# Kernel tuning notes

Measured on AMD Instinct MI355X. Metric: run time of the kernel, lower is better.

## Reference

```python
import jax, jax.numpy as jnp
import numpy as np

B, S, V, E, H, F, L = 64, 32, 10000, 512, 512, 2048, 2
D = E + H  # concat(x, h) size; embedding_size == hidden_size so all layers share shapes


def setup_inputs() -> dict:
    key = jax.random.key(0)
    ks = jax.random.split(key, 10)

    def w(k, shape, fan):
        return jax.random.normal(k, shape, jnp.float32) / jnp.sqrt(jnp.float32(fan))

    tokens = jax.random.randint(ks[0], (B, S), 0, V)
    cnn_features = jax.random.normal(ks[1], (B, F), jnp.float32)
    emb = w(ks[2], (V, E), E)
    w_in = w(ks[3], (F, H), F)
    b_in = jnp.zeros((H,), jnp.float32)
    w_r = w(ks[4], (L, D, H), D)
    b_r = jnp.zeros((L, 1, H), jnp.float32)
    w_u = w(ks[5], (L, D, H), D)
    b_u = jnp.zeros((L, 1, H), jnp.float32)
    w_h = w(ks[6], (L, D, H), D)
    b_h = jnp.zeros((L, 1, H), jnp.float32)
    w_out = w(ks[7], (H, V), H)
    b_out = jnp.zeros((V,), jnp.float32)
    return dict(tokens=tokens, cnn_features=cnn_features, emb=emb, w_in=w_in, b_in=b_in,
                w_r=w_r, b_r=b_r, w_u=w_u, b_u=b_u, w_h=w_h, b_h=b_h,
                w_out=w_out, b_out=b_out)


def reference(tokens, cnn_features, emb, w_in, b_in, w_r, b_r, w_u, b_u, w_h, b_h, w_out, b_out):
    x = emb[tokens]                                   # [B, S, E]
    h0 = cnn_features @ w_in + b_in                   # [B, H] initial hidden state from CNN features
    seq = x
    for l in range(L):
        Wr, br = w_r[l], b_r[l]
        Wu, bu = w_u[l], b_u[l]
        Wh, bh = w_h[l], b_h[l]

        def step(h, xt):
            # xt: [B, D_in], h: [B, H] -- same GRU math as GRUCell.forward, batched
            xh = jnp.concatenate([xt, h], axis=-1)
            r = jax.nn.sigmoid(xh @ Wr + br)
            h_tilde = jnp.tanh(jnp.concatenate([xt, r * h], axis=-1) @ Wh + bh)
            u = jax.nn.sigmoid(xh @ Wu + bu)
            h_new = h * u + (1.0 - u) * h_tilde
            return h_new, h_new

        _, ys = jax.lax.scan(step, h0, jnp.swapaxes(seq, 0, 1))  # scan over time
        seq = jnp.swapaxes(ys, 0, 1)                  # [B, S, H]
    logits = seq @ w_out + b_out                      # [B, S, V]
    return logits
```

## Files before the change

### kernel.cpp

```cpp
#include <hip/hip_runtime.h>
#include <hip/hip_bf16.h>

typedef __hip_bfloat16 bf16;
typedef __attribute__((ext_vector_type(8))) short bf16x8s;
typedef __attribute__((ext_vector_type(4))) float f32x4;
typedef __attribute__((ext_vector_type(4))) int i32x4;

#define NB 64
#define NS 32
#define NV 10000
#define NE 512
#define NH 512
#define NF 2048
#define ND 1024

static __device__ __forceinline__ float bf2f(bf16 x) { return __bfloat162float(x); }
static __device__ __forceinline__ bf16 f2bf(float x) { return __float2bfloat16(x); }
static __device__ __forceinline__ short bfbits(float x) { bf16 h = f2bf(x); return *(short*)&h; }
static __device__ __forceinline__ f32x4 mfma16(bf16x8s a, bf16x8s b, f32x4 c) {
  return __builtin_amdgcn_mfma_f32_16x16x32_bf16(a, b, c, 0, 0, 0);
}

static __device__ __forceinline__ i32x4 ld16_sc(const void* p) {
  i32x4 r;
  asm volatile("global_load_dwordx4 %0, %1, off sc0 sc1" : "=v"(r) : "v"(p) : "memory");
  return r;
}
static __device__ __forceinline__ void st16_sc(void* p, i32x4 v) {
  asm volatile("global_store_dwordx4 %0, %1, off sc0 sc1" :: "v"(p), "v"(v) : "memory");
}
static __device__ __forceinline__ void stud_sc(void* p, unsigned v) {
  asm volatile("global_store_dword %0, %1, off sc0 sc1" :: "v"(p), "v"(v) : "memory");
}
static __device__ __forceinline__ void wait_vm0() {
  asm volatile("s_waitcnt vmcnt(0)" ::: "memory");
  __builtin_amdgcn_sched_barrier(0);
}
static __device__ __forceinline__ unsigned min4u(i32x4 a) {
  return min(min((unsigned)a[0], (unsigned)a[1]), min((unsigned)a[2], (unsigned)a[3]));
}

__device__ __forceinline__ f32x4 wave_tile16(const bf16* A, const bf16* BT,
                                             int lda, int K, int m0, int n0) {
  int lane = threadIdx.x & 63;
  int r = lane & 15, g = lane >> 4;
  const bf16* ap = A + (size_t)(m0 + r) * lda + g * 8;
  const bf16* bp = BT + (size_t)(n0 + r) * K + g * 8;
  f32x4 acc = {0.f, 0.f, 0.f, 0.f};
#pragma unroll 4
  for (int k = 0; k < K; k += 32) {
    bf16x8s a = *(const bf16x8s*)(ap + k);
    bf16x8s b = *(const bf16x8s*)(bp + k);
    acc = mfma16(a, b, acc);
  }
  return acc;
}

__global__ void k_setup(const float* __restrict__ cnn, bf16* __restrict__ cnn_b,
                        const float* __restrict__ w_in, bf16* __restrict__ w_in_T,
                        const float* __restrict__ w_r, const float* __restrict__ w_u,
                        const float* __restrict__ w_h, bf16* __restrict__ ruhT,
                        bf16* __restrict__ hhT, bf16* __restrict__ xT,
                        const float* __restrict__ br, const float* __restrict__ bu,
                        const float* __restrict__ bh, float* __restrict__ bias) {
  const int bid = blockIdx.x;
  if (bid < 512) {
    int i = bid * 256 + threadIdx.x;
    cnn_b[i] = f2bf(cnn[i]);
    return;
  }
  if (bid < 4608) {
    const float* src; bf16* dst; int n0, k0, N;
    if (bid < 1536) {
      int b = bid - 512;
      n0 = (b & 15) * 32; k0 = (b >> 4) * 32; N = NH;
      src = w_in; dst = w_in_T;
      __shared__ float tile[32][33];
      int tx = threadIdx.x & 31, ty = threadIdx.x >> 5;
      for (int i = ty; i < 32; i += 8)
        tile[i][tx] = src[(size_t)(k0 + i) * N + n0 + tx];
      __syncthreads();
      for (int i = ty; i < 32; i += 8)
        dst[(size_t)(n0 + i) * NF + k0 + tx] = f2bf(tile[tx][i]);
      return;
    }
    int b = bid - 1536;
    int z = b >> 8, xy = b & 255;
    int l = z / 6, q = z % 6;
    const float* srcs[6] = {
      w_r + (size_t)l * ND * NH + (size_t)512 * NH,
      w_u + (size_t)l * ND * NH + (size_t)512 * NH,
      w_h + (size_t)l * ND * NH + (size_t)512 * NH,
      w_r + (size_t)l * ND * NH,
      w_u + (size_t)l * ND * NH,
      w_h + (size_t)l * ND * NH };
    bf16* dsts[6] = {
      ruhT + (size_t)l * 1024 * 512,
      ruhT + (size_t)l * 1024 * 512 + 512 * 512,
      hhT  + (size_t)l * 512 * 512,
      xT   + (size_t)l * 1536 * 512,
      xT   + (size_t)l * 1536 * 512 + 512 * 512,
      xT   + (size_t)l * 1536 * 512 + 1024 * 512 };
    src = srcs[q]; dst = dsts[q];
    n0 = (xy & 15) * 32; k0 = (xy >> 4) * 32;
    __shared__ float tile[32][33];
    int tx = threadIdx.x & 31, ty = threadIdx.x >> 5;
    for (int i = ty; i < 32; i += 8)
      tile[i][tx] = src[(size_t)(k0 + i) * NH + n0 + tx];
    __syncthreads();
    for (int i = ty; i < 32; i += 8)
      dst[(size_t)(n0 + i) * NH + k0 + tx] = f2bf(tile[tx][i]);
    return;
  }
  int i = (bid - 4608) * 256 + threadIdx.x;
  if (i < 3072) {
    int l = i / 1536, c = i % 1536;
    const float* s = (c < 512) ? (br + l * 512 + c)
                   : (c < 1024 ? (bu + l * 512 + (c - 512)) : (bh + l * 512 + (c - 1024)));
    bias[i] = *s;
  }
}

__global__ void k_gemm_h0(const bf16* __restrict__ A, const bf16* __restrict__ BT,
                          const float* __restrict__ bias,
                          float* __restrict__ h0f, bf16* __restrict__ h0b) {
  int wid = blockIdx.x * 4 + (threadIdx.x >> 6);
  int mt = wid & 3, nt = wid >> 2;
  f32x4 acc = wave_tile16(A, BT, NF, NF, mt * 16, nt * 16);
  int lane = threadIdx.x & 63;
  int cl = lane & 15, g = lane >> 4;
  int col = nt * 16 + cl;
  float bv = bias[col];
#pragma unroll
  for (int j = 0; j < 4; j++) {
    int row = mt * 16 + g * 4 + j;
    float v = acc[j] + bv;
    h0f[(size_t)row * NH + col] = v;
    h0b[(size_t)row * NH + col] = f2bf(v);
  }
}

__global__ __launch_bounds__(512, 1)
void k_gru2(const bf16* __restrict__ w_ruh, const bf16* __restrict__ w_hh,
            const bf16* __restrict__ w_x, const float* __restrict__ bias3,
            const float* __restrict__ h0f, const bf16* __restrict__ h0b,
            const int* __restrict__ tokens, const float* __restrict__ emb,
            bf16* __restrict__ seq0, bf16* __restrict__ seq1,
            bf16* __restrict__ rh_all, float* __restrict__ pre,
            unsigned* __restrict__ flags, const float* __restrict__ w_out,
            const float* __restrict__ b_out, float* __restrict__ out) {
  __shared__ char lds[40960];
  const int tid = threadIdx.x;
  const int lane = tid & 63;
  const int wv = tid >> 6;
  const int cl = lane & 15, g4 = lane >> 4;
  const int bid = blockIdx.x;
  const int in0 = lane * 16;
  const int dsw = in0 ^ ((wv & 7) << 4);

  auto stage = [&](char* dst, const char* srcbase, int rstr) {
    i32x4 v0 = ld16_sc(srcbase + (size_t)wv * rstr + in0);
    i32x4 v1 = ld16_sc(srcbase + (size_t)(wv + 8) * rstr + in0);
    wait_vm0();
    *(i32x4*)(dst + wv * 1024 + dsw) = v0;
    *(i32x4*)(dst + (wv + 8) * 1024 + dsw) = v1;
  };
  auto afrag = [&](const char* panel, int kk) {
    return *(const bf16x8s*)(panel + cl * 1024 + ((kk * 64 + g4 * 16) ^ ((cl & 7) << 4)));
  };
  auto poll8 = [&](const unsigned* f, unsigned tgt) {
    if (tid == 0) {
      for (;;) {
        i32x4 a = ld16_sc(f);
        i32x4 b = ld16_sc(f + 4);
        wait_vm0();
        if (min(min4u(a), min4u(b)) >= tgt) break;
        __builtin_amdgcn_s_sleep(1);
      }
    }
    __syncthreads();
    __builtin_amdgcn_sched_barrier(0);
  };
  auto poll32 = [&](const unsigned* f, unsigned tgt) {
    if (tid == 0) {
      for (;;) {
        i32x4 a0 = ld16_sc(f),      a1 = ld16_sc(f + 4),  a2 = ld16_sc(f + 8),
              a3 = ld16_sc(f + 12), a4 = ld16_sc(f + 16), a5 = ld16_sc(f + 20),
              a6 = ld16_sc(f + 24), a7 = ld16_sc(f + 28);
        wait_vm0();
        unsigned mn = min(min(min(min4u(a0), min4u(a1)), min(min4u(a2), min4u(a3))),
                          min(min(min4u(a4), min4u(a5)), min(min4u(a6), min4u(a7))));
        if (mn >= tgt) break;
        __builtin_amdgcn_s_sleep(1);
      }
    }
    __syncthreads();
    __builtin_amdgcn_sched_barrier(0);
  };

  if (bid < 64) {
    const int l = bid >> 5, wg5 = bid & 31, mt = wg5 & 3, ng = wg5 >> 2;
    const bool is_u = (wv >= 4);
    const int wsub = wv & 3;
    const int c = (ng * 4 + wsub) * 16 + cl;
    const int colA = is_u ? 512 + c : c;
    char* hp = lds;
    char* rp = lds + 16384;
    float* ul = (float*)(lds + 32768);
    char* rout = lds + 36864;
    char* hout = lds + 38912;

    unsigned* f_h  = flags + (l * 4 + mt) * 32;
    unsigned* f_rh = flags + 256 + (l * 4 + mt) * 32;
    unsigned* f_pre = flags + 512 + (l * 4 + mt) * 32;

    bf16* seql = l ? seq1 : seq0;
    bf16* rh = rh_all + (size_t)l * 64 * 512;
    float* prel = pre + (size_t)l * 4 * 1536 * 64;

    bf16x8s bwA[16];
    { const bf16* pa = w_ruh + (size_t)l * 1024 * 512 + (size_t)colA * NH + g4 * 8;
#pragma unroll
      for (int k = 0; k < 16; k++) bwA[k] = *(const bf16x8s*)(pa + k * 32); }
    bf16x8s bwB[16];
    float h_reg[4];
    if (!is_u) {
      const bf16* pb = w_hh + (size_t)l * 512 * 512 + (size_t)c * NH + g4 * 8;
#pragma unroll
      for (int k = 0; k < 16; k++) bwB[k] = *(const bf16x8s*)(pb + k * 32);
#pragma unroll
      for (int j = 0; j < 4; j++)
        h_reg[j] = h0f[(size_t)(mt * 16 + g4 * 4 + j) * NH + c];
    }

    for (int t = 0; t < NS; t++) {
      if (tid == 0) {
        for (;;) {
          i32x4 p0 = ld16_sc(f_pre), p1 = ld16_sc(f_pre + 4), p2 = ld16_sc(f_pre + 8);
          i32x4 h0_, h1_;
          if (t) { h0_ = ld16_sc(f_h); h1_ = ld16_sc(f_h + 4); }
          wait_vm0();
          unsigned mnp = min(min(min4u(p0), min4u(p1)), min4u(p2));
          bool ok = mnp >= (unsigned)(t + 1);
          if (t) ok = ok && (min(min4u(h0_), min4u(h1_)) >= (unsigned)t);
          if (ok) break;
          __builtin_amdgcn_s_sleep(1);
        }
      }
      __syncthreads();
      __builtin_amdgcn_sched_barrier(0);
      const int slot = t & 3;
      i32x4 pv1 = ld16_sc(prel + ((size_t)(slot * 1536 + colA) * 64 + mt * 16 + g4 * 4));
      i32x4 pv2 = {0, 0, 0, 0};
      if (!is_u)
        pv2 = ld16_sc(prel + ((size_t)(slot * 1536 + 1024 + c) * 64 + mt * 16 + g4 * 4));
      if (t == 0) stage(hp, (const char*)(h0b + (size_t)mt * 16 * NH), 1024);
      else        stage(hp, (const char*)seql + ((size_t)(mt * 16) * NS + (t - 1)) * 1024,
                        NS * 1024);
      __syncthreads();
      f32x4 pA = *(f32x4*)&pv1;
      f32x4 pB = *(f32x4*)&pv2;
      {
        f32x4 acc = {0.f, 0.f, 0.f, 0.f};
#pragma unroll
        for (int kk = 0; kk < 16; kk++) acc = mfma16(afrag(hp, kk), bwA[kk], acc);
#pragma unroll
        for (int j = 0; j < 4; j++) {
          float gate = 1.f / (1.f + expf(-(acc[j] + pA[j])));
          if (is_u) {
            ul[(g4 * 4 + j) * 64 + wsub * 16 + cl] = gate;
          } else {
            bf16 o = f2bf(gate * h_reg[j]);
            *(unsigned short*)(rout + (g4 * 4 + j) * 128 + (wsub * 16 + cl) * 2)
              = *(unsigned short*)&o;
          }
        }
      }
      __syncthreads();
      {
        if (tid < 128) {
          int row = tid >> 3, ch = tid & 7;
          i32x4 v = *(i32x4*)(rout + row * 128 + ch * 16);
          st16_sc((char*)rh + (((size_t)(mt * 16 + row)) * NH + ng * 64 + ch * 8) * 2, v);
        }
        wait_vm0();
        __syncthreads();
        if (tid == 0) stud_sc(f_rh + ng, (unsigned)(t + 1));
      }
      poll8(f_rh, (unsigned)(t + 1));
      stage(rp, (const char*)(rh + (size_t)mt * 16 * NH), 1024);
      __syncthreads();
      if (!is_u) {
        f32x4 acc = {0.f, 0.f, 0.f, 0.f};
#pragma unroll
        for (int kk = 0; kk < 16; kk++) acc = mfma16(afrag(rp, kk), bwB[kk], acc);
#pragma unroll
        for (int j = 0; j < 4; j++) {
          float htil = tanhf(acc[j] + pB[j]);
          float u = ul[(g4 * 4 + j) * 64 + wsub * 16 + cl];
          float hnew = h_reg[j] * u + (1.f - u) * htil;
          h_reg[j] = hnew;
          bf16 hn = f2bf(hnew);
          *(unsigned short*)(hout + (g4 * 4 + j) * 128 + (wsub * 16 + cl) * 2)
            = *(unsigned short*)&hn;
        }
      }
      __syncthreads();
      {
        if (tid < 128) {
          int row = tid >> 3, ch = tid & 7;
          i32x4 v = *(i32x4*)(hout + row * 128 + ch * 16);
          st16_sc((char*)seql + (((size_t)(mt * 16 + row) * NS + t) * NH + ng * 64 + ch * 8) * 2, v);
        }
        wait_vm0();
        __syncthreads();
        if (tid == 0) {
          stud_sc(f_h + ng, (unsigned)(t + 1));
          if (l == 1) stud_sc(flags + 960 + mt * 8 + ng, (unsigned)(t + 1));
        }
      }
    }
  } else if (bid < 160) {
    const int wb = bid - 64;
    const int l = wb / 48, w48 = wb % 48, gg = w48 & 3, cw = w48 >> 2;
    char* xpan = lds;
    const int col = cw * 128 + wv * 16 + cl;
    float* prel = pre + (size_t)l * 4 * 1536 * 64;
    unsigned* f_h0g = flags + (0 * 4 + gg) * 32;
    unsigned* f_own = flags + (l * 4 + gg) * 32;
    unsigned* f_out = flags + 512 + (l * 4 + gg) * 32 + cw;

    bf16x8s wxw[16];
    { const bf16* pw = w_x + (size_t)l * 1536 * 512 + (size_t)col * 512 + g4 * 8;
#pragma unroll
      for (int kk = 0; kk < 16; kk++) wxw[kk] = *(const bf16x8s*)(pw + kk * 32); }
    const float bz = bias3[l * 1536 + col];

    for (int t = 0; t < NS; t++) {
      if (l == 1 || t >= 4) {
        if (tid == 0) {
          for (;;) {
            i32x4 a0 = {0,0,0,0}, a1 = {0,0,0,0}, b0 = {0,0,0,0}, b1 = {0,0,0,0};
            if (l == 1) { a0 = ld16_sc(f_h0g); a1 = ld16_sc(f_h0g + 4); }
            if (t >= 4) { b0 = ld16_sc(f_own); b1 = ld16_sc(f_own + 4); }
            wait_vm0();
            bool ok = true;
            if (l == 1) ok = min(min4u(a0), min4u(a1)) >= (unsigned)(t + 1);
            if (t >= 4) ok = ok && (min(min4u(b0), min4u(b1)) >= (unsigned)(t - 3));
            if (ok) break;
            __builtin_amdgcn_s_sleep(1);
          }
        }
        __syncthreads();
        __builtin_amdgcn_sched_barrier(0);
      }
      if (l == 0) {
#pragma unroll
        for (int rr = 0; rr < 2; rr++) {
          int r = wv + rr * 8;
          int tok = tokens[(gg * 16 + r) * NS + t];
          const float* ep = emb + (size_t)tok * NE + lane * 8;
          f32x4 v0 = *(const f32x4*)ep;
          f32x4 v1 = *(const f32x4*)(ep + 4);
          bf16x8s o;
#pragma unroll
          for (int j = 0; j < 4; j++) { o[j] = bfbits(v0[j]); o[4 + j] = bfbits(v1[j]); }
          *(i32x4*)(xpan + r * 1024 + dsw) = *(i32x4*)&o;
        }
      } else {
        stage(xpan, (const char*)seq0 + ((size_t)(gg * 16) * NS + t) * 1024, NS * 1024);
      }
      __syncthreads();
      f32x4 acc = {0.f, 0.f, 0.f, 0.f};
#pragma unroll
      for (int kk = 0; kk < 16; kk++) acc = mfma16(afrag(xpan, kk), wxw[kk], acc);
      {
        f32x4 o;
#pragma unroll
        for (int j = 0; j < 4; j++) o[j] = acc[j] + bz;
        st16_sc(prel + ((size_t)((t & 3) * 1536 + col) * 64 + gg * 16 + g4 * 4),
                *(i32x4*)&o);
      }
      wait_vm0();
      __syncthreads();
      if (tid == 0) stud_sc(f_out, (unsigned)(t + 1));
    }
  } else {
    const int oj = bid - 160;
    const int bh = oj & 1, cg = oj >> 1;
    char* aslab = lds;
    const int colb0 = (cg * 16 + wv * 2) * 16 + cl;
    const int colb1 = colb0 + 16;
    bf16x8s bw0[16], bw1[16];
#pragma unroll
    for (int kk = 0; kk < 16; kk++) {
      bf16x8s f0, f1;
#pragma unroll
      for (int jj = 0; jj < 8; jj++) {
        int k = kk * 32 + g4 * 8 + jj;
        f0[jj] = (colb0 < NV) ? bfbits(w_out[(size_t)k * NV + colb0]) : (short)0;
        f1[jj] = (colb1 < NV) ? bfbits(w_out[(size_t)k * NV + colb1]) : (short)0;
      }
      bw0[kk] = f0; bw1[kk] = f1;
    }
    const float bz0 = (colb0 < NV) ? b_out[colb0] : 0.f;
    const float bz1 = (colb1 < NV) ? b_out[colb1] : 0.f;
    unsigned* f1f = flags + 960;

    for (int t = 0; t < NS; t++) {
      poll32(f1f, (unsigned)(t + 1));
      {
        i32x4 vv[4];
        int rows[4], offs[4];
#pragma unroll
        for (int k4 = 0; k4 < 4; k4++) {
          int chunk = k4 * 512 + tid;
          rows[k4] = chunk >> 6;
          offs[k4] = (chunk & 63) * 16;
          vv[k4] = ld16_sc((const char*)seq1 +
                           ((size_t)(bh * 32 + rows[k4]) * NS + t) * 1024 + offs[k4]);
        }
        wait_vm0();
#pragma unroll
        for (int k4 = 0; k4 < 4; k4++)
          *(i32x4*)(aslab + rows[k4] * 1024 + (offs[k4] ^ ((rows[k4] & 7) << 4))) = vv[k4];
      }
      __syncthreads();
      f32x4 acc00 = {}, acc01 = {}, acc10 = {}, acc11 = {};
#pragma unroll
      for (int kk = 0; kk < 16; kk++) {
        int r0 = cl, r1 = 16 + cl;
        bf16x8s a0 = *(const bf16x8s*)(aslab + r0 * 1024 +
                                       ((kk * 64 + g4 * 16) ^ ((r0 & 7) << 4)));
        bf16x8s a1 = *(const bf16x8s*)(aslab + r1 * 1024 +
                                       ((kk * 64 + g4 * 16) ^ ((r1 & 7) << 4)));
        acc00 = mfma16(a0, bw0[kk], acc00);
        acc01 = mfma16(a0, bw1[kk], acc01);
        acc10 = mfma16(a1, bw0[kk], acc10);
        acc11 = mfma16(a1, bw1[kk], acc11);
      }
#pragma unroll
      for (int j = 0; j < 4; j++) {
        int b0r = bh * 32 + g4 * 4 + j;
        int b1r = b0r + 16;
        if (colb0 < NV) {
          out[((size_t)b0r * NS + t) * NV + colb0] = acc00[j] + bz0;
          out[((size_t)b1r * NS + t) * NV + colb0] = acc10[j] + bz0;
        }
        if (colb1 < NV) {
          out[((size_t)b0r * NS + t) * NV + colb1] = acc01[j] + bz1;
          out[((size_t)b1r * NS + t) * NV + colb1] = acc11[j] + bz1;
        }
      }
      __syncthreads();
    }
  }
}

extern "C" void kernel_launch(void* const* d_in, const int* in_sizes, int n_in,
                              void* d_out, int out_size, void* d_ws, size_t ws_size,
                              hipStream_t stream) {
  const int*   tokens = (const int*)d_in[0];
  const float* cnn    = (const float*)d_in[1];
  const float* emb    = (const float*)d_in[2];
  const float* w_in   = (const float*)d_in[3];
  const float* b_in   = (const float*)d_in[4];
  const float* w_r    = (const float*)d_in[5];
  const float* b_r    = (const float*)d_in[6];
  const float* w_u    = (const float*)d_in[7];
  const float* b_u    = (const float*)d_in[8];
  const float* w_h    = (const float*)d_in[9];
  const float* b_h    = (const float*)d_in[10];
  const float* w_out  = (const float*)d_in[11];
  const float* b_out  = (const float*)d_in[12];
  float* out = (float*)d_out;

  char* ws = (char*)d_ws;
  size_t off = 0;
  auto alloc = [&](size_t bytes) { char* p = ws + off; off += (bytes + 255) & ~(size_t)255; return p; };
  bf16*  seq0    = (bf16*) alloc((size_t)2048 * 512 * 2);
  bf16*  seq1    = (bf16*) alloc((size_t)2048 * 512 * 2);
  float* pre     = (float*)alloc((size_t)2 * 4 * 1536 * 64 * 4);
  float* h0f     = (float*)alloc((size_t)64 * 512 * 4);
  bf16*  h0b     = (bf16*) alloc((size_t)64 * 512 * 2);
  bf16*  rh_all  = (bf16*) alloc((size_t)2 * 64 * 512 * 2);
  float* bias3   = (float*)alloc((size_t)2 * 1536 * 4);
  bf16*  cnn_b   = (bf16*) alloc((size_t)64 * 2048 * 2);
  bf16*  w_in_T  = (bf16*) alloc((size_t)512 * 2048 * 2);
  bf16*  w_ruh_T = (bf16*) alloc((size_t)2 * 1024 * 512 * 2);
  bf16*  w_hh_T  = (bf16*) alloc((size_t)2 * 512 * 512 * 2);
  bf16*  w_x_T   = (bf16*) alloc((size_t)2 * 1536 * 512 * 2);
  unsigned* flags = (unsigned*)alloc(4096);
  (void)ws_size; (void)in_sizes; (void)n_in; (void)out_size;

  hipMemsetAsync(flags, 0, 4096, stream);

  k_setup<<<4620, 256, 0, stream>>>(cnn, cnn_b, w_in, w_in_T, w_r, w_u, w_h,
                                    w_ruh_T, w_hh_T, w_x_T, b_r, b_u, b_h, bias3);
  k_gemm_h0<<<32, 256, 0, stream>>>(cnn_b, w_in_T, b_in, h0f, h0b);
  k_gru2<<<256, 512, 0, stream>>>(w_ruh_T, w_hh_T, w_x_T, bias3, h0f, h0b,
                                  tokens, emb, seq0, seq1, rh_all, pre, flags,
                                  w_out, b_out, out);
}
```

Before: 232.0 us.

## Repartition GRU recurrence to fewer workgroups, each wave computing r, u and h-tilde

The recurrent part now runs on 32 workgroups instead of 64. Each wave computes all three gates for 16 columns, keeping the u gate in registers, which removes the LDS exchange between the r/u waves and the h waves. The u-gate weights are reloaded from global memory on every step, and outputs are written as individual 2-byte stores instead of being staged through LDS into 16-byte stores. Flag polling shrinks to match the smaller group counts, the grid drops to 224 blocks, and launch bounds and LDS size change. The trade-off is fewer cross-block flag handshakes per step against more global traffic and more serial MFMA work per wave.

```diff
diff --git a/kernel.cpp b/kernel.cpp
--- a/kernel.cpp
+++ b/kernel.cpp
@@ -31,6 +31,9 @@
 }
 static __device__ __forceinline__ void stud_sc(void* p, unsigned v) {
   asm volatile("global_store_dword %0, %1, off sc0 sc1" :: "v"(p), "v"(v) : "memory");
+}
+static __device__ __forceinline__ void stus_sc(void* p, unsigned v) {
+  asm volatile("global_store_short %0, %1, off sc0 sc1" :: "v"(p), "v"(v) : "memory");
 }
 static __device__ __forceinline__ void wait_vm0() {
   asm volatile("s_waitcnt vmcnt(0)" ::: "memory");
@@ -70,15 +73,15 @@
     return;
   }
   if (bid < 4608) {
-    const float* src; bf16* dst; int n0, k0, N;
+    const float* src; bf16* dst; int n0, k0;
     if (bid < 1536) {
       int b = bid - 512;
-      n0 = (b & 15) * 32; k0 = (b >> 4) * 32; N = NH;
+      n0 = (b & 15) * 32; k0 = (b >> 4) * 32;
       src = w_in; dst = w_in_T;
       __shared__ float tile[32][33];
       int tx = threadIdx.x & 31, ty = threadIdx.x >> 5;
       for (int i = ty; i < 32; i += 8)
-        tile[i][tx] = src[(size_t)(k0 + i) * N + n0 + tx];
+        tile[i][tx] = src[(size_t)(k0 + i) * NH + n0 + tx];
       __syncthreads();
       for (int i = ty; i < 32; i += 8)
         dst[(size_t)(n0 + i) * NF + k0 + tx] = f2bf(tile[tx][i]);
@@ -140,7 +143,7 @@
   }
 }
 
-__global__ __launch_bounds__(512, 1)
+__global__ __launch_bounds__(512, 2)
 void k_gru2(const bf16* __restrict__ w_ruh, const bf16* __restrict__ w_hh,
             const bf16* __restrict__ w_x, const float* __restrict__ bias3,
             const float* __restrict__ h0f, const bf16* __restrict__ h0b,
@@ -149,7 +152,7 @@
             bf16* __restrict__ rh_all, float* __restrict__ pre,
             unsigned* __restrict__ flags, const float* __restrict__ w_out,
             const float* __restrict__ b_out, float* __restrict__ out) {
-  __shared__ char lds[40960];
+  __shared__ char lds[32768];
   const int tid = threadIdx.x;
   const int lane = tid & 63;
   const int wv = tid >> 6;
@@ -168,28 +171,24 @@
   auto afrag = [&](const char* panel, int kk) {
     return *(const bf16x8s*)(panel + cl * 1024 + ((kk * 64 + g4 * 16) ^ ((cl & 7) << 4)));
   };
-  auto poll8 = [&](const unsigned* f, unsigned tgt) {
+  auto poll4 = [&](const unsigned* f, unsigned tgt) {
     if (tid == 0) {
       for (;;) {
         i32x4 a = ld16_sc(f);
-        i32x4 b = ld16_sc(f + 4);
         wait_vm0();
-        if (min(min4u(a), min4u(b)) >= tgt) break;
+        if (min4u(a) >= tgt) break;
         __builtin_amdgcn_s_sleep(1);
       }
     }
     __syncthreads();
     __builtin_amdgcn_sched_barrier(0);
   };
-  auto poll32 = [&](const unsigned* f, unsigned tgt) {
+  auto poll16 = [&](const unsigned* f, unsigned tgt) {
     if (tid == 0) {
       for (;;) {
-        i32x4 a0 = ld16_sc(f),      a1 = ld16_sc(f + 4),  a2 = ld16_sc(f + 8),
-              a3 = ld16_sc(f + 12), a4 = ld16_sc(f + 16), a5 = ld16_sc(f + 20),
-              a6 = ld16_sc(f + 24), a7 = ld16_sc(f + 28);
+        i32x4 a0 = ld16_sc(f), a1 = ld16_sc(f + 4), a2 = ld16_sc(f + 8), a3 = ld16_sc(f + 12);
         wait_vm0();
-        unsigned mn = min(min(min(min4u(a0), min4u(a1)), min(min4u(a2), min4u(a3))),
-                          min(min(min4u(a4), min4u(a5)), min(min4u(a6), min4u(a7))));
+        unsigned mn = min(min(min4u(a0), min4u(a1)), min(min4u(a2), min4u(a3)));
         if (mn >= tgt) break;
         __builtin_amdgcn_s_sleep(1);
       }
@@ -198,17 +197,11 @@
     __builtin_amdgcn_sched_barrier(0);
   };
 
-  if (bid < 64) {
-    const int l = bid >> 5, wg5 = bid & 31, mt = wg5 & 3, ng = wg5 >> 2;
-    const bool is_u = (wv >= 4);
-    const int wsub = wv & 3;
-    const int c = (ng * 4 + wsub) * 16 + cl;
-    const int colA = is_u ? 512 + c : c;
+  if (bid < 32) {
+    const int l = bid >> 4, r4 = bid & 15, mt = r4 & 3, q = r4 >> 2;
+    const int c = q * 128 + wv * 16 + cl;
     char* hp = lds;
     char* rp = lds + 16384;
-    float* ul = (float*)(lds + 32768);
-    char* rout = lds + 36864;
-    char* hout = lds + 38912;
 
     unsigned* f_h  = flags + (l * 4 + mt) * 32;
     unsigned* f_rh = flags + 256 + (l * 4 + mt) * 32;
@@ -218,31 +211,31 @@
     bf16* rh = rh_all + (size_t)l * 64 * 512;
     float* prel = pre + (size_t)l * 4 * 1536 * 64;
 
-    bf16x8s bwA[16];
-    { const bf16* pa = w_ruh + (size_t)l * 1024 * 512 + (size_t)colA * NH + g4 * 8;
-#pragma unroll
-      for (int k = 0; k < 16; k++) bwA[k] = *(const bf16x8s*)(pa + k * 32); }
-    bf16x8s bwB[16];
+    bf16x8s bwR[16];
+    { const bf16* pa = w_ruh + (size_t)l * 1024 * 512 + (size_t)c * NH + g4 * 8;
+#pragma unroll
+      for (int k = 0; k < 16; k++) bwR[k] = *(const bf16x8s*)(pa + k * 32); }
+    bf16x8s bwH[16];
+    { const bf16* pb = w_hh + (size_t)l * 512 * 512 + (size_t)c * NH + g4 * 8;
+#pragma unroll
+      for (int k = 0; k < 16; k++) bwH[k] = *(const bf16x8s*)(pb + k * 32); }
+    const bf16* wu_ptr = w_ruh + (size_t)l * 1024 * 512 + (size_t)(512 + c) * NH + g4 * 8;
+
     float h_reg[4];
-    if (!is_u) {
-      const bf16* pb = w_hh + (size_t)l * 512 * 512 + (size_t)c * NH + g4 * 8;
-#pragma unroll
-      for (int k = 0; k < 16; k++) bwB[k] = *(const bf16x8s*)(pb + k * 32);
-#pragma unroll
-      for (int j = 0; j < 4; j++)
-        h_reg[j] = h0f[(size_t)(mt * 16 + g4 * 4 + j) * NH + c];
-    }
+#pragma unroll
+    for (int j = 0; j < 4; j++)
+      h_reg[j] = h0f[(size_t)(mt * 16 + g4 * 4 + j) * NH + c];
 
     for (int t = 0; t < NS; t++) {
       if (tid == 0) {
         for (;;) {
           i32x4 p0 = ld16_sc(f_pre), p1 = ld16_sc(f_pre + 4), p2 = ld16_sc(f_pre + 8);
-          i32x4 h0_, h1_;
-          if (t) { h0_ = ld16_sc(f_h); h1_ = ld16_sc(f_h + 4); }
+          i32x4 hh = {0, 0, 0, 0};
+          if (t) hh = ld16_sc(f_h);
           wait_vm0();
           unsigned mnp = min(min(min4u(p0), min4u(p1)), min4u(p2));
           bool ok = mnp >= (unsigned)(t + 1);
-          if (t) ok = ok && (min(min4u(h0_), min4u(h1_)) >= (unsigned)t);
+          if (t) ok = ok && (min4u(hh) >= (unsigned)t);
           if (ok) break;
           __builtin_amdgcn_s_sleep(1);
         }
@@ -250,78 +243,67 @@
       __syncthreads();
       __builtin_amdgcn_sched_barrier(0);
       const int slot = t & 3;
-      i32x4 pv1 = ld16_sc(prel + ((size_t)(slot * 1536 + colA) * 64 + mt * 16 + g4 * 4));
-      i32x4 pv2 = {0, 0, 0, 0};
-      if (!is_u)
-        pv2 = ld16_sc(prel + ((size_t)(slot * 1536 + 1024 + c) * 64 + mt * 16 + g4 * 4));
+      i32x4 pvR = ld16_sc(prel + ((size_t)(slot * 1536 + c) * 64 + mt * 16 + g4 * 4));
+      i32x4 pvU = ld16_sc(prel + ((size_t)(slot * 1536 + 512 + c) * 64 + mt * 16 + g4 * 4));
+      i32x4 pvB = ld16_sc(prel + ((size_t)(slot * 1536 + 1024 + c) * 64 + mt * 16 + g4 * 4));
       if (t == 0) stage(hp, (const char*)(h0b + (size_t)mt * 16 * NH), 1024);
       else        stage(hp, (const char*)seql + ((size_t)(mt * 16) * NS + (t - 1)) * 1024,
                         NS * 1024);
       __syncthreads();
-      f32x4 pA = *(f32x4*)&pv1;
-      f32x4 pB = *(f32x4*)&pv2;
+      f32x4 pR = *(f32x4*)&pvR;
+      f32x4 pU = *(f32x4*)&pvU;
+      f32x4 pB = *(f32x4*)&pvB;
       {
         f32x4 acc = {0.f, 0.f, 0.f, 0.f};
 #pragma unroll
-        for (int kk = 0; kk < 16; kk++) acc = mfma16(afrag(hp, kk), bwA[kk], acc);
+        for (int kk = 0; kk < 16; kk++) acc = mfma16(afrag(hp, kk), bwR[kk], acc);
 #pragma unroll
         for (int j = 0; j < 4; j++) {
-          float gate = 1.f / (1.f + expf(-(acc[j] + pA[j])));
-          if (is_u) {
-            ul[(g4 * 4 + j) * 64 + wsub * 16 + cl] = gate;
-          } else {
-            bf16 o = f2bf(gate * h_reg[j]);
-            *(unsigned short*)(rout + (g4 * 4 + j) * 128 + (wsub * 16 + cl) * 2)
-              = *(unsigned short*)&o;
-          }
-        }
-      }
-      __syncthreads();
+          float gate = 1.f / (1.f + expf(-(acc[j] + pR[j])));
+          int b = mt * 16 + g4 * 4 + j;
+          bf16 o = f2bf(gate * h_reg[j]);
+          stus_sc((void*)(rh + (size_t)b * NH + c), *(unsigned short*)&o);
+        }
+      }
+      float u_reg[4];
       {
-        if (tid < 128) {
-          int row = tid >> 3, ch = tid & 7;
-          i32x4 v = *(i32x4*)(rout + row * 128 + ch * 16);
-          st16_sc((char*)rh + (((size_t)(mt * 16 + row)) * NH + ng * 64 + ch * 8) * 2, v);
-        }
-        wait_vm0();
-        __syncthreads();
-        if (tid == 0) stud_sc(f_rh + ng, (unsigned)(t + 1));
-      }
-      poll8(f_rh, (unsigned)(t + 1));
-      stage(rp, (const char*)(rh + (size_t)mt * 16 * NH), 1024);
-      __syncthreads();
-      if (!is_u) {
         f32x4 acc = {0.f, 0.f, 0.f, 0.f};
 #pragma unroll
-        for (int kk = 0; kk < 16; kk++) acc = mfma16(afrag(rp, kk), bwB[kk], acc);
+        for (int kk = 0; kk < 16; kk++)
+          acc = mfma16(afrag(hp, kk), *(const bf16x8s*)(wu_ptr + kk * 32), acc);
+#pragma unroll
+        for (int j = 0; j < 4; j++)
+          u_reg[j] = 1.f / (1.f + expf(-(acc[j] + pU[j])));
+      }
+      wait_vm0();
+      __syncthreads();
+      if (tid == 0) stud_sc(f_rh + q, (unsigned)(t + 1));
+      poll4(f_rh, (unsigned)(t + 1));
+      stage(rp, (const char*)rh + (size_t)mt * 16 * 1024, 1024);
+      __syncthreads();
+      {
+        f32x4 acc = {0.f, 0.f, 0.f, 0.f};
+#pragma unroll
+        for (int kk = 0; kk < 16; kk++) acc = mfma16(afrag(rp, kk), bwH[kk], acc);
 #pragma unroll
         for (int j = 0; j < 4; j++) {
           float htil = tanhf(acc[j] + pB[j]);
-          float u = ul[(g4 * 4 + j) * 64 + wsub * 16 + cl];
-          float hnew = h_reg[j] * u + (1.f - u) * htil;
+          float hnew = h_reg[j] * u_reg[j] + (1.f - u_reg[j]) * htil;
           h_reg[j] = hnew;
           bf16 hn = f2bf(hnew);
-          *(unsigned short*)(hout + (g4 * 4 + j) * 128 + (wsub * 16 + cl) * 2)
-            = *(unsigned short*)&hn;
-        }
-      }
-      __syncthreads();
-      {
-        if (tid < 128) {
-          int row = tid >> 3, ch = tid & 7;
-          i32x4 v = *(i32x4*)(hout + row * 128 + ch * 16);
-          st16_sc((char*)seql + (((size_t)(mt * 16 + row) * NS + t) * NH + ng * 64 + ch * 8) * 2, v);
-        }
-        wait_vm0();
-        __syncthreads();
-        if (tid == 0) {
-          stud_sc(f_h + ng, (unsigned)(t + 1));
-          if (l == 1) stud_sc(flags + 960 + mt * 8 + ng, (unsigned)(t + 1));
-        }
-      }
-    }
-  } else if (bid < 160) {
-    const int wb = bid - 64;
+          int b = mt * 16 + g4 * 4 + j;
+          stus_sc((void*)(seql + ((size_t)b * NS + t) * NH + c), *(unsigned short*)&hn);
+        }
+      }
+      wait_vm0();
+      __syncthreads();
+      if (tid == 0) {
+        stud_sc(f_h + q, (unsigned)(t + 1));
+        if (l == 1) stud_sc(flags + 960 + mt * 4 + q, (unsigned)(t + 1));
+      }
+    }
+  } else if (bid < 128) {
+    const int wb = bid - 32;
     const int l = wb / 48, w48 = wb % 48, gg = w48 & 3, cw = w48 >> 2;
     char* xpan = lds;
     const int col = cw * 128 + wv * 16 + cl;
@@ -340,13 +322,13 @@
       if (l == 1 || t >= 4) {
         if (tid == 0) {
           for (;;) {
-            i32x4 a0 = {0,0,0,0}, a1 = {0,0,0,0}, b0 = {0,0,0,0}, b1 = {0,0,0,0};
-            if (l == 1) { a0 = ld16_sc(f_h0g); a1 = ld16_sc(f_h0g + 4); }
-            if (t >= 4) { b0 = ld16_sc(f_own); b1 = ld16_sc(f_own + 4); }
+            i32x4 a0 = {0,0,0,0}, b0 = {0,0,0,0};
+            if (l == 1) a0 = ld16_sc(f_h0g);
+            if (t >= 4) b0 = ld16_sc(f_own);
             wait_vm0();
             bool ok = true;
-            if (l == 1) ok = min(min4u(a0), min4u(a1)) >= (unsigned)(t + 1);
-            if (t >= 4) ok = ok && (min(min4u(b0), min4u(b1)) >= (unsigned)(t - 3));
+            if (l == 1) ok = min4u(a0) >= (unsigned)(t + 1);
+            if (t >= 4) ok = ok && (min4u(b0) >= (unsigned)(t - 3));
             if (ok) break;
             __builtin_amdgcn_s_sleep(1);
           }
@@ -386,7 +368,7 @@
       if (tid == 0) stud_sc(f_out, (unsigned)(t + 1));
     }
   } else {
-    const int oj = bid - 160;
+    const int oj = bid - 128;
     const int bh = oj & 1, cg = oj >> 1;
     char* aslab = lds;
     const int colb0 = (cg * 16 + wv * 2) * 16 + cl;
@@ -408,7 +390,7 @@
     unsigned* f1f = flags + 960;
 
     for (int t = 0; t < NS; t++) {
-      poll32(f1f, (unsigned)(t + 1));
+      poll16(f1f, (unsigned)(t + 1));
       {
         i32x4 vv[4];
         int rows[4], offs[4];
@@ -498,7 +480,7 @@
   k_setup<<<4620, 256, 0, stream>>>(cnn, cnn_b, w_in, w_in_T, w_r, w_u, w_h,
                                     w_ruh_T, w_hh_T, w_x_T, b_r, b_u, b_h, bias3);
   k_gemm_h0<<<32, 256, 0, stream>>>(cnn_b, w_in_T, b_in, h0f, h0b);
-  k_gru2<<<256, 512, 0, stream>>>(w_ruh_T, w_hh_T, w_x_T, bias3, h0f, h0b,
+  k_gru2<<<224, 512, 0, stream>>>(w_ruh_T, w_hh_T, w_x_T, bias3, h0f, h0b,
                                   tokens, emb, seq0, seq1, rh_all, pre, flags,
                                   w_out, b_out, out);
 }
```

Result: slower. 347.9 us (+49.9%).
